# Kernel optimization log

Hardware: AMD Instinct MI355X
Metric: run time of the kernel (lower is better)

The kernel has to match this reference:

```python
import jax, jax.numpy as jnp
import numpy as np

LAYERS, DIM, FFN, HEADS = 2, 1024, 4096, 8
HD = DIM // HEADS          # head qk dim = 128
VD = DIM                   # v_dim (double_v_dim=False)
HV = VD // HEADS           # head v dim = 128
B, L = 2, 2048
SCALE_BASE = 512.0
EPS = 1e-5


def setup_inputs() -> dict:
    key = jax.random.key(0)
    ks = jax.random.split(key, 18)
    def rn(k, shape, s=1.0):
        return jax.random.normal(k, shape, dtype=jnp.float32) * s
    return dict(
        X=rn(ks[0], (B, L, DIM)),
        Wq=rn(ks[1], (LAYERS, HEADS, DIM, HD), 1.0 / DIM),
        Wk=rn(ks[2], (LAYERS, HEADS, DIM, HD), 1.0 / DIM),
        Wv=rn(ks[3], (LAYERS, HEADS, DIM, HV), 1.0 / DIM),
        W_G=rn(ks[4], (LAYERS, DIM, VD), 1.0 / DIM),
        W_O=rn(ks[5], (LAYERS, VD, DIM), 1.0 / DIM),
        gn_w=1.0 + 0.02 * rn(ks[6], (LAYERS, VD)),
        gn_b=0.02 * rn(ks[7], (LAYERS, VD)),
        ln1_w=1.0 + 0.02 * rn(ks[8], (LAYERS, DIM)),
        ln1_b=0.02 * rn(ks[9], (LAYERS, DIM)),
        ln2_w=1.0 + 0.02 * rn(ks[10], (LAYERS, DIM)),
        ln2_b=0.02 * rn(ks[11], (LAYERS, DIM)),
        ffn_w1=rn(ks[12], (LAYERS, DIM, FFN), DIM ** -0.5),
        ffn_b1=0.02 * rn(ks[13], (LAYERS, FFN)),
        ffn_w2=rn(ks[14], (LAYERS, FFN, DIM), FFN ** -0.5),
        ffn_b2=0.02 * rn(ks[15], (LAYERS, DIM)),
    )


def _xpos_tables(length, head_dim):
    half = head_dim // 2
    pos = jnp.arange(length, dtype=jnp.float32)
    base_scale = (jnp.arange(0, head_dim, 2, dtype=jnp.float32) + 0.4 * head_dim) / (1.4 * head_dim)
    sc = base_scale[None, :] ** (pos / SCALE_BASE)[:, None]          # [L, half]
    inv_freq = 1.0 / (10000.0 ** (jnp.arange(half, dtype=jnp.float32) / half))
    ang = pos[:, None] * inv_freq[None, :]                           # [L, half]
    return sc, jnp.sin(ang), jnp.cos(ang)


def _dup(t):
    # duplicate_interleave: [L, half] -> [L, head_dim]
    return jnp.repeat(t, 2, axis=-1)


def _rotate_every_two(x):
    x1, x2 = x[..., ::2], x[..., 1::2]
    return jnp.stack([-x2, x1], axis=-1).reshape(x.shape)


def _apply_xpos(x, sc, sin, cos, downscale):
    s = 1.0 / sc if downscale else sc
    return x * _dup(cos * s) + _rotate_every_two(x) * _dup(sin * s)


def _layernorm(x, w, b):
    mu = jnp.mean(x, axis=-1, keepdims=True)
    var = jnp.var(x, axis=-1, keepdims=True)
    return (x - mu) * jax.lax.rsqrt(var + EPS) * w + b


def _decay_matrix(length):
    gammas = jnp.asarray(1.0 - np.exp(np.linspace(np.log(1 / 32), np.log(1 / 512), HEADS)), dtype=jnp.float32)
    n = jnp.arange(length, dtype=jnp.float32)
    delta = n[:, None] - n[None, :]                                  # [L, L]
    logg = jnp.log(gammas)[:, None, None]                            # [H, 1, 1]
    return jnp.where(delta[None] >= 0, jnp.exp(logg * delta[None]), 0.0)  # [H, L, L]


def _msr(X, Wq, Wk, Wv, gn_w, gn_b, W_G, W_O, D, sc, sin, cos):
    b, l, d = X.shape
    Q = _apply_xpos(jnp.einsum('bld,hde->bhle', X, Wq), sc, sin, cos, False)
    K = _apply_xpos(jnp.einsum('bld,hde->bhle', X, Wk), sc, sin, cos, True)
    V = jnp.einsum('bld,hdv->bhlv', X, Wv)
    scores = jnp.einsum('bhle,bhme->bhlm', Q, K) * D[None]           # [B,H,L,L] decayed
    Y = jnp.einsum('bhlm,bhmv->bhlv', scores, V)                     # [B,H,L,HV]
    # GroupNorm(heads, v_dim) over per-token concatenated heads == per-head norm
    mu = jnp.mean(Y, axis=-1, keepdims=True)
    var = jnp.var(Y, axis=-1, keepdims=True)
    Yn = (Y - mu) * jax.lax.rsqrt(var + EPS)
    Yn = Yn * gn_w.reshape(HEADS, 1, HV)[None] + gn_b.reshape(HEADS, 1, HV)[None]
    Yc = jnp.transpose(Yn, (0, 2, 1, 3)).reshape(b, l, VD)
    G = X @ W_G
    gate = G * jax.nn.sigmoid(G)                                     # swish
    return (gate * Yc) @ W_O


def reference(X, Wq, Wk, Wv, W_G, W_O, gn_w, gn_b, ln1_w, ln1_b, ln2_w, ln2_b, ffn_w1, ffn_b1, ffn_w2, ffn_b2):
    l = X.shape[1]
    sc, sin, cos = _xpos_tables(l, HD)
    D = _decay_matrix(l)
    for i in range(LAYERS):
        Y = _msr(_layernorm(X, ln1_w[i], ln1_b[i]), Wq[i], Wk[i], Wv[i],
                 gn_w[i], gn_b[i], W_G[i], W_O[i], D, sc, sin, cos) + X
        h = _layernorm(Y, ln2_w[i], ln2_b[i])
        h = jax.nn.gelu(h @ ffn_w1[i] + ffn_b1[i], approximate=False)
        X = h @ ffn_w2[i] + ffn_b2[i] + Y                            # Dropout is identity in eval
    return X
```

## Files before the change

### kernel.cpp

```cpp
#include <hip/hip_runtime.h>
#include <math.h>

#define DIM 1024
#define FFN_DIM 4096
#define HEADS 8
#define HD 128
#define BB 2
#define LL 2048
#define NROWS (BB*LL)

typedef __attribute__((ext_vector_type(8))) short bf16x8;
typedef __attribute__((ext_vector_type(4))) short bf16x4;
typedef __attribute__((ext_vector_type(2))) short bf16x2;
typedef __attribute__((ext_vector_type(4))) float f32x4;

__device__ inline short f2bf(float f) {
    unsigned u = __builtin_bit_cast(unsigned, f);
    unsigned r = (u + 0x7FFFu + ((u >> 16) & 1u)) >> 16;
    return (short)r;
}
__device__ inline float bf2f(short s) {
    unsigned u = ((unsigned)(unsigned short)s) << 16;
    return __builtin_bit_cast(float, u);
}

__device__ __forceinline__ void gl_lds16(const void* g, void* l) {
    __builtin_amdgcn_global_load_lds(
        (const __attribute__((address_space(1))) unsigned int*)g,
        (__attribute__((address_space(3))) unsigned int*)l, 16, 0, 0);
}

__global__ __launch_bounds__(256) void ln_kernel_bf(
    const float* __restrict__ x, const float* __restrict__ w,
    const float* __restrict__ b, short* __restrict__ out)
{
    int row = blockIdx.x;
    int tid = threadIdx.x;
    const float* xr = x + (size_t)row * DIM;
    float4 v = *(const float4*)(xr + tid * 4);
    float s  = v.x + v.y + v.z + v.w;
    float ss = v.x*v.x + v.y*v.y + v.z*v.z + v.w*v.w;
    #pragma unroll
    for (int o = 32; o > 0; o >>= 1) { s += __shfl_down(s, o); ss += __shfl_down(ss, o); }
    __shared__ float red[10];
    int wid = tid >> 6;
    if ((tid & 63) == 0) { red[wid] = s; red[4 + wid] = ss; }
    __syncthreads();
    if (tid == 0) {
        float t  = red[0] + red[1] + red[2] + red[3];
        float t2 = red[4] + red[5] + red[6] + red[7];
        float mu  = t * (1.f / DIM);
        float var = t2 * (1.f / DIM) - mu * mu;
        red[8] = mu; red[9] = rsqrtf(var + 1e-5f);
    }
    __syncthreads();
    float mu = red[8], rs = red[9];
    float4 wv = *(const float4*)(w + tid * 4);
    float4 bv = *(const float4*)(b + tid * 4);
    bf16x4 o;
    o[0] = f2bf((v.x - mu) * rs * wv.x + bv.x);
    o[1] = f2bf((v.y - mu) * rs * wv.y + bv.y);
    o[2] = f2bf((v.z - mu) * rs * wv.z + bv.z);
    o[3] = f2bf((v.w - mu) * rs * wv.w + bv.w);
    *(bf16x4*)(out + (size_t)row * DIM + tid * 4) = o;
}

__global__ __launch_bounds__(256) void transpose_cvt(
    const float* __restrict__ in, short* __restrict__ out,
    int R, int C, size_t ibs, size_t obs)
{
    __shared__ float t[32][33];
    int bz = blockIdx.z;
    int r0 = blockIdx.y * 32, c0 = blockIdx.x * 32;
    int tx = threadIdx.x & 31, ty = threadIdx.x >> 5;
    const float* ip = in + (size_t)bz * ibs;
    short* op = out + (size_t)bz * obs;
    #pragma unroll
    for (int i = 0; i < 4; ++i)
        t[ty + i * 8][tx] = ip[(size_t)(r0 + ty + i * 8) * C + c0 + tx];
    __syncthreads();
    #pragma unroll
    for (int i = 0; i < 4; ++i)
        op[(size_t)(c0 + ty + i * 8) * R + r0 + tx] = f2bf(t[tx][ty + i * 8]);
}

__global__ __launch_bounds__(256) void vt_cvt(
    const short* __restrict__ Vb, short* __restrict__ Vt)
{
    __shared__ short t[32][34];
    int r0 = blockIdx.y * 32, c0 = blockIdx.x * 32;
    int tx = threadIdx.x & 31, ty = threadIdx.x >> 5;
    #pragma unroll
    for (int i = 0; i < 4; ++i)
        t[ty + i * 8][tx] = Vb[(size_t)(r0 + ty + i * 8) * DIM + c0 + tx];
    __syncthreads();
    int b = r0 >> 11;
    int l = (r0 & (LL - 1));
    #pragma unroll
    for (int i = 0; i < 4; ++i) {
        int c = c0 + ty + i * 8;
        int h = c >> 7, v = c & 127;
        Vt[(((size_t)(b * HEADS + h) * HD + v) << 11) + l + tx] = t[tx][ty + i * 8];
    }
}

template<int EPI, int GX>
__global__ __launch_bounds__(256) void gemm_bf16(
    const short* __restrict__ A, const short* __restrict__ Bt,
    void* __restrict__ Cv, const float* __restrict__ bias,
    const float* __restrict__ R_,
    void* __restrict__ P1, void* __restrict__ P2, void* __restrict__ P3,
    int N, int K, int M)
{
    __shared__ __align__(16) short As[2][128 * 32];
    __shared__ __align__(16) short Bs[2][128 * 32];
    int tid = threadIdx.x;
    int w = tid >> 6, lane = tid & 63;
    int q = lane >> 4, lr = lane & 15;
    int wr = w >> 1, wc = w & 1;

    int id = blockIdx.y * GX + blockIdx.x;
    int xcd = id & 7, j = id >> 3;
    constexpr int rx_n = (GX >= 8) ? GX / 8 : 1;
    int tp = (GX * gridDim.y) >> 3;
    int rh = tp >> 3;
    int lbx = j & 7, lby = j >> 3;
    int rx = xcd % rx_n, ry = xcd / rx_n;
    int bm = (ry * rh + lby) * 128;
    int bn = (rx * 8 + lbx) * 128;

    int srow = lane >> 2;
    int sseg = lane & 3;

    f32x4 acc[4][4];
    #pragma unroll
    for (int mi = 0; mi < 4; ++mi)
        #pragma unroll
        for (int ni = 0; ni < 4; ++ni) acc[mi][ni] = (f32x4){0.f, 0.f, 0.f, 0.f};

    #pragma unroll
    for (int i = 0; i < 2; ++i) {
        int jj = w * 2 + i;
        int row = jj * 16 + srow;
        int cseg = sseg ^ ((row >> 1) & 3);
        gl_lds16(A  + (size_t)(bm + row) * K + cseg * 8, &As[0][jj * 16 * 32]);
        gl_lds16(Bt + (size_t)(bn + row) * K + cseg * 8, &Bs[0][jj * 16 * 32]);
    }

    int nk = K >> 5;
    for (int kt = 0; kt < nk; ++kt) {
        int cur = kt & 1;
        __syncthreads();
        if (kt + 1 < nk) {
            int k1 = (kt + 1) << 5;
            #pragma unroll
            for (int i = 0; i < 2; ++i) {
                int jj = w * 2 + i;
                int row = jj * 16 + srow;
                int cseg = sseg ^ ((row >> 1) & 3);
                gl_lds16(A  + (size_t)(bm + row) * K + k1 + cseg * 8, &As[cur ^ 1][jj * 16 * 32]);
                gl_lds16(Bt + (size_t)(bn + row) * K + k1 + cseg * 8, &Bs[cur ^ 1][jj * 16 * 32]);
            }
        }
        bf16x8 af[4], bfr[4];
        #pragma unroll
        for (int mi = 0; mi < 4; ++mi) {
            int row = wr * 64 + mi * 16 + lr;
            af[mi] = *(const bf16x8*)&As[cur][row * 32 + (q ^ ((row >> 1) & 3)) * 8];
        }
        #pragma unroll
        for (int ni = 0; ni < 4; ++ni) {
            int row = wc * 64 + ni * 16 + lr;
            bfr[ni] = *(const bf16x8*)&Bs[cur][row * 32 + (q ^ ((row >> 1) & 3)) * 8];
        }
        #pragma unroll
        for (int mi = 0; mi < 4; ++mi)
            #pragma unroll
            for (int ni = 0; ni < 4; ++ni)
                acc[mi][ni] = __builtin_amdgcn_mfma_f32_16x16x32_bf16(af[mi], bfr[ni], acc[mi][ni], 0, 0, 0);
    }

    if constexpr (EPI == 4) {
        int sel = bn >> 10;
        int row_base = bm + wr * 64 + q * 4;
        int l0 = row_base & (LL - 1);
        #pragma unroll
        for (int ni = 0; ni < 4; ++ni) {
            int col = bn + wc * 64 + ni * 16 + lr;
            int cq = col & (DIM - 1);
            if (sel <= 1) {
                int jj = (col & 127) >> 1;
                float lb = log2f((2.f * jj + 51.2f) / 179.2f);
                if (sel == 1) lb = -lb;
                float invf = exp2f(-(float)jj * (13.287712379549449f / 64.f));
                float snb, cnb;
                sincosf((float)l0 * invf, &snb, &cnb);
                float scb = exp2f(lb * (float)l0 * (1.f / 512.f));
                float s1, c1, s16, c16;
                __sincosf(invf, &s1, &c1);
                __sincosf(16.f * invf, &s16, &c16);
                float st1 = exp2f(lb * (1.f / 512.f));
                float st16 = exp2f(lb * (16.f / 512.f));
                short* Ob = (short*)(sel == 0 ? Cv : P1);
                #pragma unroll
                for (int mi = 0; mi < 4; ++mi) {
                    float cr = cnb, sr = snb, sv = scb;
                    #pragma unroll
                    for (int r = 0; r < 4; ++r) {
                        float cs = cr * sv, ssn = sr * sv;
                        float v = acc[mi][ni][r];
                        float p = __shfl_xor(v, 1);
                        float o = (lr & 1) ? (v * cs + p * ssn) : (v * cs - p * ssn);
                        Ob[(size_t)(row_base + mi * 16 + r) * DIM + cq] = f2bf(o);
                        if (r < 3) {
                            float crn = cr * c1 - sr * s1;
                            sr = sr * c1 + cr * s1; cr = crn;
                            sv *= st1;
                        }
                    }
                    float cbn = cnb * c16 - snb * s16;
                    snb = snb * c16 + cnb * s16; cnb = cbn;
                    scb *= st16;
                }
            } else if (sel == 2) {
                short* Vb = (short*)P2;
                #pragma unroll
                for (int mi = 0; mi < 4; ++mi)
                    #pragma unroll
                    for (int r = 0; r < 4; ++r)
                        Vb[(size_t)(row_base + mi * 16 + r) * DIM + cq] = f2bf(acc[mi][ni][r]);
            } else {
                short* Gb = (short*)P3;
                #pragma unroll
                for (int mi = 0; mi < 4; ++mi)
                    #pragma unroll
                    for (int r = 0; r < 4; ++r)
                        Gb[(size_t)(row_base + mi * 16 + r) * DIM + cq] = f2bf(acc[mi][ni][r]);
            }
        }
        return;
    }

    float* Cf = (float*)Cv;
    short* Cs = (short*)Cv;
    #pragma unroll
    for (int ni = 0; ni < 4; ++ni) {
        int col = bn + wc * 64 + ni * 16 + lr;
        float bi = 0.f;
        if constexpr (EPI == 1 || EPI == 2) bi = bias[col];
        #pragma unroll
        for (int mi = 0; mi < 4; ++mi) {
            int row0 = bm + wr * 64 + mi * 16 + q * 4;
            #pragma unroll
            for (int r = 0; r < 4; ++r) {
                size_t off = (size_t)(row0 + r) * M + col;
                float v = acc[mi][ni][r];
                if constexpr (EPI == 1) {
                    v += bi;
                    v = 0.5f * v * (1.f + erff(v * 0.70710678118654752f));
                    Cs[off] = f2bf(v);
                } else if constexpr (EPI == 2) {
                    Cf[off] = v + bi + R_[off];
                } else if constexpr (EPI == 3) {
                    Cf[off] = v + R_[off];
                } else {
                    Cf[off] = v;
                }
            }
        }
    }
}

#define PSTR 40
__global__ __launch_bounds__(256) void retention_mfma2(
    const short* __restrict__ Qb, const short* __restrict__ Kb,
    const short* __restrict__ Vt, float* __restrict__ Y)
{
    __shared__ __align__(16) short Ks[2][32 * 128];
    __shared__ __align__(16) short Vs[2][128 * 32];
    __shared__ __align__(16) short Ps[4][16 * PSTR];
    int tid = threadIdx.x;
    int w = tid >> 6, lane = tid & 63;
    int q = lane >> 4, lr = lane & 15;
    int bh = blockIdx.x;
    int b = bh >> 3, h = bh & 7;
    size_t bL = (size_t)b * LL;
    const short* Kbh = Kb + (bL << 10) + (h << 7);
    const short* Qbh = Qb + (bL << 10) + (h << 7);
    const short* Vbh = Vt + ((size_t)bh << 18);
    float* Ybh = Y + (bL << 10) + (h << 7);

    const float lg_lo = -3.4657359027997265f;
    const float lg_hi = -6.2383246250395075f;
    float gamma = 1.f - expf(lg_lo + (lg_hi - lg_lo) * ((float)h / 7.f));
    float logg = logf(gamma);
    float gm32 = expf(-32.f * logg);
    float rf[4];
    #pragma unroll
    for (int r = 0; r < 4; ++r) rf[r] = expf(logg * (float)(q * 4 + r));
    float cf0 = expf(-logg * (float)lr);
    float cf1 = expf(-logg * (float)(16 + lr));
    int dqlr = q * 4 - lr;

    int krow = lane >> 4;
    int kslot = lane & 15;
    int vrow = lane >> 2;
    int vslot = lane & 3;

    #pragma unroll 1
    for (int pass = 0; pass < 2; ++pass) {
        int jt = pass ? (31 - blockIdx.y) : blockIdx.y;
        int l0w = jt * 64 + w * 16;
        int ntiles = 2 * jt + 2;

        bf16x8 qf[4];
        {
            const short* qp = Qbh + ((size_t)(l0w + lr) << 10) + q * 8;
            #pragma unroll
            for (int es = 0; es < 4; ++es) qf[es] = *(const bf16x8*)(qp + es * 32);
        }
        f32x4 yacc[8];
        #pragma unroll
        for (int vt = 0; vt < 8; ++vt) yacc[vt] = (f32x4){0.f, 0.f, 0.f, 0.f};
        float tf = expf(logg * (float)l0w);

        #pragma unroll
        for (int i = 0; i < 2; ++i) {
            int kr = w * 8 + i * 4 + krow;
            gl_lds16(Kbh + ((size_t)kr << 10) + ((kslot ^ (kr & 15)) << 3),
                     &Ks[0][(w * 8 + i * 4) * 128]);
            int vr = w * 32 + i * 16 + vrow;
            gl_lds16(Vbh + ((size_t)vr << 11) + ((vslot ^ (vr & 3)) << 3),
                     &Vs[0][(w * 32 + i * 16) * 32]);
        }

        #pragma unroll 1
        for (int mt = 0; mt < ntiles; ++mt) {
            int cur = mt & 1;
            int m0 = mt * 32;
            __syncthreads();
            if (mt + 1 < ntiles) {
                int m1 = m0 + 32;
                #pragma unroll
                for (int i = 0; i < 2; ++i) {
                    int kr = w * 8 + i * 4 + krow;
                    gl_lds16(Kbh + ((size_t)(m1 + kr) << 10) + ((kslot ^ (kr & 15)) << 3),
                             &Ks[cur ^ 1][(w * 8 + i * 4) * 128]);
                    int vr = w * 32 + i * 16 + vrow;
                    gl_lds16(Vbh + ((size_t)vr << 11) + m1 + ((vslot ^ (vr & 3)) << 3),
                             &Vs[cur ^ 1][(w * 32 + i * 16) * 32]);
                }
            }
            if (m0 <= l0w + 15) {
                int dt = l0w - m0;
                f32x4 sa0 = (f32x4){0.f,0.f,0.f,0.f};
                f32x4 sa1 = (f32x4){0.f,0.f,0.f,0.f};
                #pragma unroll
                for (int es = 0; es < 4; ++es) {
                    int slot = ((es * 4 + q) ^ lr) * 8;
                    bf16x8 bk0 = *(const bf16x8*)&Ks[cur][lr * 128 + slot];
                    bf16x8 bk1 = *(const bf16x8*)&Ks[cur][(16 + lr) * 128 + slot];
                    sa0 = __builtin_amdgcn_mfma_f32_16x16x32_bf16(qf[es], bk0, sa0, 0, 0, 0);
                    sa1 = __builtin_amdgcn_mfma_f32_16x16x32_bf16(qf[es], bk1, sa1, 0, 0, 0);
                }
                #pragma unroll
                for (int r = 0; r < 4; ++r) {
                    float p0 = sa0[r] * (rf[r] * cf0 * tf);
                    float p1 = sa1[r] * (rf[r] * cf1 * tf);
                    int d0 = dt + dqlr + r;
                    Ps[w][(q*4 + r) * PSTR + lr]      = (d0 >= 0)      ? f2bf(p0) : (short)0;
                    Ps[w][(q*4 + r) * PSTR + 16 + lr] = (d0 - 16 >= 0) ? f2bf(p1) : (short)0;
                }
                bf16x8 pa = *(const bf16x8*)&Ps[w][lr * PSTR + q * 8];
                int vslot_r = (q ^ (lr & 3)) * 8;
                #pragma unroll
                for (int vt = 0; vt < 8; ++vt) {
                    bf16x8 bv = *(const bf16x8*)&Vs[cur][(vt * 16 + lr) * 32 + vslot_r];
                    yacc[vt] = __builtin_amdgcn_mfma_f32_16x16x32_bf16(pa, bv, yacc[vt], 0, 0, 0);
                }
            }
            tf *= gm32;
        }
        __syncthreads();
        float* yp = Ybh + ((size_t)(l0w + q * 4) << 10) + lr;
        #pragma unroll
        for (int vt = 0; vt < 8; ++vt)
            #pragma unroll
            for (int r = 0; r < 4; ++r)
                yp[((size_t)r << 10) + vt * 16] = yacc[vt][r];
    }
}

__global__ __launch_bounds__(256) void gn_gate_kernel(
    const float* __restrict__ Y, const short* __restrict__ Gb,
    const float* __restrict__ w, const float* __restrict__ b,
    short* __restrict__ ybf)
{
    int tid = threadIdx.x;
    int wid = tid >> 6, lane = tid & 63;
    int grp = blockIdx.x * 4 + wid;
    int n = grp >> 3, h = grp & 7;
    size_t base = (size_t)n * DIM + h * HD + lane * 2;
    float2 y = *(const float2*)(Y + base);
    float s = y.x + y.y, ss = y.x * y.x + y.y * y.y;
    #pragma unroll
    for (int o = 32; o > 0; o >>= 1) { s += __shfl_down(s, o); ss += __shfl_down(ss, o); }
    s = __shfl(s, 0); ss = __shfl(ss, 0);
    float mu  = s * (1.f / HD);
    float var = ss * (1.f / HD) - mu * mu;
    float rs  = rsqrtf(var + 1e-5f);
    float2 wv = *(const float2*)(w + h * HD + lane * 2);
    float2 bv = *(const float2*)(b + h * HD + lane * 2);
    bf16x2 gv = *(const bf16x2*)(Gb + base);
    float gx = bf2f(gv[0]), gy = bf2f(gv[1]);
    float g0 = gx / (1.f + expf(-gx));
    float g1 = gy / (1.f + expf(-gy));
    bf16x2 o;
    o[0] = f2bf(((y.x - mu) * rs * wv.x + bv.x) * g0);
    o[1] = f2bf(((y.y - mu) * rs * wv.y + bv.y) * g1);
    *(bf16x2*)(ybf + base) = o;
}

extern "C" void kernel_launch(void* const* d_in, const int* in_sizes, int n_in,
                              void* d_out, int out_size, void* d_ws, size_t ws_size,
                              hipStream_t stream)
{
    const float* X0   = (const float*)d_in[0];
    const float* Wq   = (const float*)d_in[1];
    const float* Wk   = (const float*)d_in[2];
    const float* Wv   = (const float*)d_in[3];
    const float* WG   = (const float*)d_in[4];
    const float* WO   = (const float*)d_in[5];
    const float* gnw  = (const float*)d_in[6];
    const float* gnb  = (const float*)d_in[7];
    const float* ln1w = (const float*)d_in[8];
    const float* ln1b = (const float*)d_in[9];
    const float* ln2w = (const float*)d_in[10];
    const float* ln2b = (const float*)d_in[11];
    const float* fw1  = (const float*)d_in[12];
    const float* fb1  = (const float*)d_in[13];
    const float* fw2  = (const float*)d_in[14];
    const float* fb2  = (const float*)d_in[15];

    float* ws = (float*)d_ws;
    const size_t U = (size_t)NROWS * DIM;

    short* lnbf  = (short*)(ws + 0 * U);
    short* wqkvg = lnbf + (size_t)NROWS * DIM;
    short* Vt   = (short*)(ws + 1 * U);
    short* fw1t = (short*)(ws + 1 * U);
    short* fw2t = fw1t + (size_t)DIM * FFN_DIM;
    float* sY  = ws + 2 * U;
    short* h1   = (short*)(ws + 2 * U);
    short* Vb   = (short*)(ws + 3 * U);
    short* ybf  = (short*)(ws + 3 * U);
    short* wot  = ybf + (size_t)NROWS * DIM;
    short* Gb   = (short*)(ws + 4 * U);
    float* sXn = ws + 4 * U;
    short* Qb   = (short*)(ws + 5 * U);
    short* Kb   = Qb + (size_t)NROWS * DIM;
    float* sX  = ws + 6 * U;

    for (int i = 0; i < 2; ++i) {
        const float* Xin = (i == 0) ? X0 : sX;
        float* Xout = (i == 1) ? (float*)d_out : sX;

        ln_kernel_bf<<<NROWS, 256, 0, stream>>>(Xin, ln1w + i * DIM, ln1b + i * DIM, lnbf);
        dim3 tq(HD / 32, DIM / 32, HEADS);
        transpose_cvt<<<tq, 256, 0, stream>>>(Wq + (size_t)i * HEADS * DIM * HD, wqkvg + 0 * DIM * DIM, DIM, HD, (size_t)DIM * HD, (size_t)HD * DIM);
        transpose_cvt<<<tq, 256, 0, stream>>>(Wk + (size_t)i * HEADS * DIM * HD, wqkvg + 1 * DIM * DIM, DIM, HD, (size_t)DIM * HD, (size_t)HD * DIM);
        transpose_cvt<<<tq, 256, 0, stream>>>(Wv + (size_t)i * HEADS * DIM * HD, wqkvg + 2 * DIM * DIM, DIM, HD, (size_t)DIM * HD, (size_t)HD * DIM);
        dim3 tg(DIM / 32, DIM / 32, 1);
        transpose_cvt<<<tg, 256, 0, stream>>>(WG + (size_t)i * DIM * DIM, wqkvg + 3 * (size_t)DIM * DIM, DIM, DIM, 0, 0);
        dim3 gp4(4 * DIM / 128, NROWS / 128);
        gemm_bf16<4, 32><<<gp4, 256, 0, stream>>>(lnbf, wqkvg, Qb, nullptr, nullptr, Kb, Vb, Gb, NROWS, DIM, 4 * DIM);
        dim3 vg(DIM / 32, NROWS / 32);
        vt_cvt<<<vg, 256, 0, stream>>>(Vb, Vt);
        dim3 rg(16, 16);
        retention_mfma2<<<rg, 256, 0, stream>>>(Qb, Kb, Vt, sY);
        gn_gate_kernel<<<NROWS * HEADS / 4, 256, 0, stream>>>(sY, Gb, gnw + i * DIM, gnb + i * DIM, ybf);
        transpose_cvt<<<tg, 256, 0, stream>>>(WO + (size_t)i * DIM * DIM, wot, DIM, DIM, 0, 0);
        dim3 gp(DIM / 128, NROWS / 128);
        gemm_bf16<3, 8><<<gp, 256, 0, stream>>>(ybf, wot, sXn, nullptr, Xin, nullptr, nullptr, nullptr, NROWS, DIM, DIM);
        ln_kernel_bf<<<NROWS, 256, 0, stream>>>(sXn, ln2w + i * DIM, ln2b + i * DIM, lnbf);
        dim3 t1(FFN_DIM / 32, DIM / 32, 1);
        transpose_cvt<<<t1, 256, 0, stream>>>(fw1 + (size_t)i * DIM * FFN_DIM, fw1t, DIM, FFN_DIM, 0, 0);
        dim3 t2(DIM / 32, FFN_DIM / 32, 1);
        transpose_cvt<<<t2, 256, 0, stream>>>(fw2 + (size_t)i * FFN_DIM * DIM, fw2t, FFN_DIM, DIM, 0, 0);
        dim3 gf1(FFN_DIM / 128, NROWS / 128);
        gemm_bf16<1, 32><<<gf1, 256, 0, stream>>>(lnbf, fw1t, h1, fb1 + i * FFN_DIM, nullptr, nullptr, nullptr, nullptr, NROWS, DIM, FFN_DIM);
        dim3 gf2(DIM / 128, NROWS / 128);
        gemm_bf16<2, 8><<<gf2, 256, 0, stream>>>(h1, fw2t, Xout, fb2 + i * DIM, sXn, nullptr, nullptr, nullptr, NROWS, FFN_DIM, DIM);
    }
}
```

Measured before the change: 837.1 us.

## Replace GEMM with 8-wave pipelined kernel using larger tiles and K=64 steps

Replaces the 4-wave 128x128 bf16 GEMM with a templated 512-thread kernel that uses K=64 stages and an 8-row XOR swizzle. It splits the A and B prefetch around two MFMA half-steps, using explicit vmcnt waits, raw barriers and s_setprio to overlap global-to-LDS loads with compute. The QKVG and FFN1 GEMMs move to 256x256 tiles, and the smaller-N GEMMs use 128x128 tiles with 8 waves. The aim is to hide memory latency and improve data reuse per block. In exchange, per-thread register and LDS use rise, and the hand-tuned waitcnt counts are fragile.

Result: faster. 799.6 us (-4.5%).

```diff
diff --git a/kernel.cpp b/kernel.cpp
--- a/kernel.cpp
+++ b/kernel.cpp
@@ -104,20 +104,24 @@
     }
 }
 
-template<int EPI, int GX>
-__global__ __launch_bounds__(256) void gemm_bf16(
+template<int EPI, int MI, int NI, int GX>
+__global__ __launch_bounds__(512, 2) void gemm_pipe(
     const short* __restrict__ A, const short* __restrict__ Bt,
     void* __restrict__ Cv, const float* __restrict__ bias,
     const float* __restrict__ R_,
     void* __restrict__ P1, void* __restrict__ P2, void* __restrict__ P3,
     int N, int K, int M)
 {
-    __shared__ __align__(16) short As[2][128 * 32];
-    __shared__ __align__(16) short Bs[2][128 * 32];
+    constexpr int BM = 32 * MI;
+    constexpr int BN = 64 * NI;
+    constexpr int LA = BM / 64;
+    constexpr int LB = BN / 64;
+    __shared__ __align__(16) short As[2][BM * 64];
+    __shared__ __align__(16) short Bs[2][BN * 64];
     int tid = threadIdx.x;
     int w = tid >> 6, lane = tid & 63;
     int q = lane >> 4, lr = lane & 15;
-    int wr = w >> 1, wc = w & 1;
+    int wr = w >> 2, wc = w & 3;
 
     int id = blockIdx.y * GX + blockIdx.x;
     int xcd = id & 7, j = id >> 3;
@@ -126,67 +130,96 @@
     int rh = tp >> 3;
     int lbx = j & 7, lby = j >> 3;
     int rx = xcd % rx_n, ry = xcd / rx_n;
-    int bm = (ry * rh + lby) * 128;
-    int bn = (rx * 8 + lbx) * 128;
-
-    int srow = lane >> 2;
-    int sseg = lane & 3;
-
-    f32x4 acc[4][4];
-    #pragma unroll
-    for (int mi = 0; mi < 4; ++mi)
-        #pragma unroll
-        for (int ni = 0; ni < 4; ++ni) acc[mi][ni] = (f32x4){0.f, 0.f, 0.f, 0.f};
-
-    #pragma unroll
-    for (int i = 0; i < 2; ++i) {
-        int jj = w * 2 + i;
-        int row = jj * 16 + srow;
-        int cseg = sseg ^ ((row >> 1) & 3);
-        gl_lds16(A  + (size_t)(bm + row) * K + cseg * 8, &As[0][jj * 16 * 32]);
-        gl_lds16(Bt + (size_t)(bn + row) * K + cseg * 8, &Bs[0][jj * 16 * 32]);
-    }
-
-    int nk = K >> 5;
+    int bm = (ry * rh + lby) * BM;
+    int bn = (rx * 8 + lbx) * BN;
+
+    int srow = tid >> 3;
+    int sseg = tid & 7;
+
+    f32x4 acc[MI][NI];
+    #pragma unroll
+    for (int mi = 0; mi < MI; ++mi)
+        #pragma unroll
+        for (int ni = 0; ni < NI; ++ni) acc[mi][ni] = (f32x4){0.f, 0.f, 0.f, 0.f};
+
+    auto stageA = [&](int bb, int k0) {
+        #pragma unroll
+        for (int i = 0; i < LA; ++i) {
+            int row = i * 64 + srow;
+            gl_lds16(A + (size_t)(bm + row) * K + k0 + ((sseg ^ (row & 7)) << 3),
+                     &As[bb][(i * 512 + tid) * 8]);
+        }
+    };
+    auto stageB = [&](int bb, int k0) {
+        #pragma unroll
+        for (int i = 0; i < LB; ++i) {
+            int row = i * 64 + srow;
+            gl_lds16(Bt + (size_t)(bn + row) * K + k0 + ((sseg ^ (row & 7)) << 3),
+                     &Bs[bb][(i * 512 + tid) * 8]);
+        }
+    };
+
+    stageA(0, 0);
+    stageB(0, 0);
+
+    int aoff = (wr * (BM / 2) + lr) * 64;
+    int boff = (wc * (BN / 4) + lr) * 64;
+    int seg0 = ((q ^ (lr & 7)) << 3);
+    int seg1 = (((4 + q) ^ (lr & 7)) << 3);
+
+    int nk = K >> 6;
+    #pragma unroll 1
     for (int kt = 0; kt < nk; ++kt) {
-        int cur = kt & 1;
-        __syncthreads();
+        int b = kt & 1;
         if (kt + 1 < nk) {
-            int k1 = (kt + 1) << 5;
+            stageA(b ^ 1, (kt + 1) << 6);
+            if constexpr (LA == 4)
+                asm volatile("s_waitcnt vmcnt(4)\ns_barrier" ::: "memory");
+            else
+                asm volatile("s_waitcnt vmcnt(2)\ns_barrier" ::: "memory");
+        } else {
+            asm volatile("s_waitcnt vmcnt(0)\ns_barrier" ::: "memory");
+        }
+        const short* as = As[b];
+        const short* bs = Bs[b];
+        bf16x8 af[MI], bfr[NI];
+        #pragma unroll
+        for (int mi = 0; mi < MI; ++mi)
+            af[mi] = *(const bf16x8*)&as[aoff + mi * 1024 + seg0];
+        #pragma unroll
+        for (int ni = 0; ni < NI; ++ni)
+            bfr[ni] = *(const bf16x8*)&bs[boff + ni * 1024 + seg0];
+        __builtin_amdgcn_s_setprio(1);
+        #pragma unroll
+        for (int mi = 0; mi < MI; ++mi)
             #pragma unroll
-            for (int i = 0; i < 2; ++i) {
-                int jj = w * 2 + i;
-                int row = jj * 16 + srow;
-                int cseg = sseg ^ ((row >> 1) & 3);
-                gl_lds16(A  + (size_t)(bm + row) * K + k1 + cseg * 8, &As[cur ^ 1][jj * 16 * 32]);
-                gl_lds16(Bt + (size_t)(bn + row) * K + k1 + cseg * 8, &Bs[cur ^ 1][jj * 16 * 32]);
-            }
-        }
-        bf16x8 af[4], bfr[4];
-        #pragma unroll
-        for (int mi = 0; mi < 4; ++mi) {
-            int row = wr * 64 + mi * 16 + lr;
-            af[mi] = *(const bf16x8*)&As[cur][row * 32 + (q ^ ((row >> 1) & 3)) * 8];
-        }
-        #pragma unroll
-        for (int ni = 0; ni < 4; ++ni) {
-            int row = wc * 64 + ni * 16 + lr;
-            bfr[ni] = *(const bf16x8*)&Bs[cur][row * 32 + (q ^ ((row >> 1) & 3)) * 8];
-        }
-        #pragma unroll
-        for (int mi = 0; mi < 4; ++mi)
+            for (int ni = 0; ni < NI; ++ni)
+                acc[mi][ni] = __builtin_amdgcn_mfma_f32_16x16x32_bf16(af[mi], bfr[ni], acc[mi][ni], 0, 0, 0);
+        __builtin_amdgcn_s_setprio(0);
+        if (kt + 1 < nk) stageB(b ^ 1, (kt + 1) << 6);
+        #pragma unroll
+        for (int mi = 0; mi < MI; ++mi)
+            af[mi] = *(const bf16x8*)&as[aoff + mi * 1024 + seg1];
+        #pragma unroll
+        for (int ni = 0; ni < NI; ++ni)
+            bfr[ni] = *(const bf16x8*)&bs[boff + ni * 1024 + seg1];
+        __builtin_amdgcn_s_setprio(1);
+        #pragma unroll
+        for (int mi = 0; mi < MI; ++mi)
             #pragma unroll
-            for (int ni = 0; ni < 4; ++ni)
+            for (int ni = 0; ni < NI; ++ni)
                 acc[mi][ni] = __builtin_amdgcn_mfma_f32_16x16x32_bf16(af[mi], bfr[ni], acc[mi][ni], 0, 0, 0);
+        __builtin_amdgcn_s_setprio(0);
+        asm volatile("s_barrier" ::: "memory");
     }
 
     if constexpr (EPI == 4) {
         int sel = bn >> 10;
-        int row_base = bm + wr * 64 + q * 4;
+        int row_base = bm + wr * (BM / 2) + q * 4;
         int l0 = row_base & (LL - 1);
         #pragma unroll
-        for (int ni = 0; ni < 4; ++ni) {
-            int col = bn + wc * 64 + ni * 16 + lr;
+        for (int ni = 0; ni < NI; ++ni) {
+            int col = bn + wc * (BN / 4) + ni * 16 + lr;
             int cq = col & (DIM - 1);
             if (sel <= 1) {
                 int jj = (col & 127) >> 1;
@@ -203,7 +236,7 @@
                 float st16 = exp2f(lb * (16.f / 512.f));
                 short* Ob = (short*)(sel == 0 ? Cv : P1);
                 #pragma unroll
-                for (int mi = 0; mi < 4; ++mi) {
+                for (int mi = 0; mi < MI; ++mi) {
                     float cr = cnb, sr = snb, sv = scb;
                     #pragma unroll
                     for (int r = 0; r < 4; ++r) {
@@ -225,14 +258,14 @@
             } else if (sel == 2) {
                 short* Vb = (short*)P2;
                 #pragma unroll
-                for (int mi = 0; mi < 4; ++mi)
+                for (int mi = 0; mi < MI; ++mi)
                     #pragma unroll
                     for (int r = 0; r < 4; ++r)
                         Vb[(size_t)(row_base + mi * 16 + r) * DIM + cq] = f2bf(acc[mi][ni][r]);
             } else {
                 short* Gb = (short*)P3;
                 #pragma unroll
-                for (int mi = 0; mi < 4; ++mi)
+                for (int mi = 0; mi < MI; ++mi)
                     #pragma unroll
                     for (int r = 0; r < 4; ++r)
                         Gb[(size_t)(row_base + mi * 16 + r) * DIM + cq] = f2bf(acc[mi][ni][r]);
@@ -244,13 +277,13 @@
     float* Cf = (float*)Cv;
     short* Cs = (short*)Cv;
     #pragma unroll
-    for (int ni = 0; ni < 4; ++ni) {
-        int col = bn + wc * 64 + ni * 16 + lr;
+    for (int ni = 0; ni < NI; ++ni) {
+        int col = bn + wc * (BN / 4) + ni * 16 + lr;
         float bi = 0.f;
         if constexpr (EPI == 1 || EPI == 2) bi = bias[col];
         #pragma unroll
-        for (int mi = 0; mi < 4; ++mi) {
-            int row0 = bm + wr * 64 + mi * 16 + q * 4;
+        for (int mi = 0; mi < MI; ++mi) {
+            int row0 = bm + wr * (BM / 2) + mi * 16 + q * 4;
             #pragma unroll
             for (int r = 0; r < 4; ++r) {
                 size_t off = (size_t)(row0 + r) * M + col;
@@ -472,8 +505,8 @@
         transpose_cvt<<<tq, 256, 0, stream>>>(Wv + (size_t)i * HEADS * DIM * HD, wqkvg + 2 * DIM * DIM, DIM, HD, (size_t)DIM * HD, (size_t)HD * DIM);
         dim3 tg(DIM / 32, DIM / 32, 1);
         transpose_cvt<<<tg, 256, 0, stream>>>(WG + (size_t)i * DIM * DIM, wqkvg + 3 * (size_t)DIM * DIM, DIM, DIM, 0, 0);
-        dim3 gp4(4 * DIM / 128, NROWS / 128);
-        gemm_bf16<4, 32><<<gp4, 256, 0, stream>>>(lnbf, wqkvg, Qb, nullptr, nullptr, Kb, Vb, Gb, NROWS, DIM, 4 * DIM);
+        dim3 gp4(4 * DIM / 256, NROWS / 256);
+        gemm_pipe<4, 8, 4, 16><<<gp4, 512, 0, stream>>>(lnbf, wqkvg, Qb, nullptr, nullptr, Kb, Vb, Gb, NROWS, DIM, 4 * DIM);
         dim3 vg(DIM / 32, NROWS / 32);
         vt_cvt<<<vg, 256, 0, stream>>>(Vb, Vt);
         dim3 rg(16, 16);
@@ -481,15 +514,15 @@
         gn_gate_kernel<<<NROWS * HEADS / 4, 256, 0, stream>>>(sY, Gb, gnw + i * DIM, gnb + i * DIM, ybf);
         transpose_cvt<<<tg, 256, 0, stream>>>(WO + (size_t)i * DIM * DIM, wot, DIM, DIM, 0, 0);
         dim3 gp(DIM / 128, NROWS / 128);
-        gemm_bf16<3, 8><<<gp, 256, 0, stream>>>(ybf, wot, sXn, nullptr, Xin, nullptr, nullptr, nullptr, NROWS, DIM, DIM);
+        gemm_pipe<3, 4, 2, 8><<<gp, 512, 0, stream>>>(ybf, wot, sXn, nullptr, Xin, nullptr, nullptr, nullptr, NROWS, DIM, DIM);
         ln_kernel_bf<<<NROWS, 256, 0, stream>>>(sXn, ln2w + i * DIM, ln2b + i * DIM, lnbf);
         dim3 t1(FFN_DIM / 32, DIM / 32, 1);
         transpose_cvt<<<t1, 256, 0, stream>>>(fw1 + (size_t)i * DIM * FFN_DIM, fw1t, DIM, FFN_DIM, 0, 0);
         dim3 t2(DIM / 32, FFN_DIM / 32, 1);
         transpose_cvt<<<t2, 256, 0, stream>>>(fw2 + (size_t)i * FFN_DIM * DIM, fw2t, FFN_DIM, DIM, 0, 0);
-        dim3 gf1(FFN_DIM / 128, NROWS / 128);
-        gemm_bf16<1, 32><<<gf1, 256, 0, stream>>>(lnbf, fw1t, h1, fb1 + i * FFN_DIM, nullptr, nullptr, nullptr, nullptr, NROWS, DIM, FFN_DIM);
+        dim3 gf1(FFN_DIM / 256, NROWS / 256);
+        gemm_pipe<1, 8, 4, 16><<<gf1, 512, 0, stream>>>(lnbf, fw1t, h1, fb1 + i * FFN_DIM, nullptr, nullptr, nullptr, nullptr, NROWS, DIM, FFN_DIM);
         dim3 gf2(DIM / 128, NROWS / 128);
-        gemm_bf16<2, 8><<<gf2, 256, 0, stream>>>(h1, fw2t, Xout, fb2 + i * DIM, sXn, nullptr, nullptr, nullptr, NROWS, FFN_DIM, DIM);
-    }
-}
+        gemm_pipe<2, 4, 2, 8><<<gf2, 512, 0, stream>>>(h1, fw2t, Xout, fb2 + i * DIM, sXn, nullptr, nullptr, nullptr, NROWS, FFN_DIM, DIM);
+    }
+}
```
